# Performance work log

Hardware: AMD Instinct MI355X
Metric: run time of the kernel (lower is better)

## Reference

```python
import jax, jax.numpy as jnp
import numpy as np

N = 4096      # mesh nodes (seq len)
D = 512       # input_dim_nodes / hidden_size
F = 512       # ffn_hidden_size (hidden_dim)
NH = 4        # num_attention_heads
HD = D // NH  # head dim = 128
L = 2         # processor_layers
EPS = 1e-5
SCALE = 1.0 / float(np.sqrt(HD))
NEG = -1e9


def setup_inputs() -> dict:
    key = jax.random.key(0)
    ks = jax.random.split(key, 16)
    nfeat = jax.random.normal(ks[0], (N, D), jnp.float32)
    # sparse graph adjacency mask: True = masked out (TE 'arbitrary' convention)
    mask = jax.random.uniform(ks[1], (N, N)) < 0.99
    idx = jnp.arange(N)
    mask = mask.at[idx, idx].set(False)  # keep self-edges unmasked
    s = 0.02
    p = lambda k, shape: jax.random.normal(k, shape, jnp.float32) * s
    return dict(
        nfeat=nfeat, mask=mask,
        ln1_g=jnp.ones((L, D), jnp.float32), ln1_b=jnp.zeros((L, D), jnp.float32),
        wq=p(ks[2], (L, D, D)), bq=p(ks[3], (L, D)),
        wk=p(ks[4], (L, D, D)), bk=p(ks[5], (L, D)),
        wv=p(ks[6], (L, D, D)), bv=p(ks[7], (L, D)),
        wo=p(ks[8], (L, D, D)), bo=p(ks[9], (L, D)),
        ln2_g=jnp.ones((L, D), jnp.float32), ln2_b=jnp.zeros((L, D), jnp.float32),
        fc1_w=p(ks[10], (L, F, D)), fc1_b=p(ks[11], (L, F)),
        fc2_w=p(ks[12], (L, D, F)), fc2_b=p(ks[13], (L, D)),
    )


def _ln(x, g, b):
    mu = x.mean(-1, keepdims=True)
    var = ((x - mu) ** 2).mean(-1, keepdims=True)
    return (x - mu) * jax.lax.rsqrt(var + EPS) * g + b


def reference(nfeat, mask, ln1_g, ln1_b, wq, bq, wk, bk, wv, bv, wo, bo,
              ln2_g, ln2_b, fc1_w, fc1_b, fc2_w, fc2_b):
    def layer(x, p):
        g1, b1, Wq, Bq, Wk, Bk, Wv, Bv, Wo, Bo, g2, b2, W1, B1, W2, B2 = p
        # --- pre-LN self-attention with arbitrary mask ---
        h = _ln(x, g1, b1)                                  # [N, D]
        q = (h @ Wq.T + Bq).reshape(N, NH, HD)
        k = (h @ Wk.T + Bk).reshape(N, NH, HD)
        v = (h @ Wv.T + Bv).reshape(N, NH, HD)
        scores = jnp.einsum('qhd,khd->hqk', q, k) * SCALE   # [NH, N, N]
        scores = jnp.where(mask[None], NEG, scores)
        attn = jax.nn.softmax(scores, axis=-1)
        o = jnp.einsum('hqk,khd->qhd', attn, v).reshape(N, D)
        x = x + o @ Wo.T + Bo
        # --- pre-LN MLP ---
        h2 = _ln(x, g2, b2)
        m = jax.nn.gelu(h2 @ W1.T + B1, approximate=False) @ W2.T + B2
        return x + m, None

    xs = (ln1_g, ln1_b, wq, bq, wk, bk, wv, bv, wo, bo,
          ln2_g, ln2_b, fc1_w, fc1_b, fc2_w, fc2_b)
    out, _ = jax.lax.scan(layer, nfeat, xs)
    return out
```

## Files before the change

kernel.cpp:

```cpp
#include <hip/hip_runtime.h>
#include <math.h>

#define NN 4096
#define DD 512
#define FF 512
#define CAP 256
#define SCALE 0.08838834764831845f

typedef unsigned short u16;
typedef __attribute__((ext_vector_type(8))) short short8;
typedef __attribute__((ext_vector_type(8))) unsigned short ushort8;
typedef __attribute__((ext_vector_type(4))) unsigned short ushort4v;
typedef __attribute__((ext_vector_type(4))) float floatx4;

__device__ __forceinline__ float bf2f(u16 u) {
    union { unsigned int i; float f; } x; x.i = ((unsigned int)u) << 16; return x.f;
}
__device__ __forceinline__ u16 f2bf(float f) {
    union { float f; unsigned int i; } x; x.f = f;
    unsigned int r = (x.i + 0x7FFFu + ((x.i >> 16) & 1u)) >> 16;
    return (u16)r;
}
__device__ __forceinline__ void gld_lds16(const void* g, void* l) {
    __builtin_amdgcn_global_load_lds((const __attribute__((address_space(1))) void*)g,
                                     (__attribute__((address_space(3))) void*)l, 16, 0, 0);
}

__global__ void build_idx_kernel(const int* __restrict__ mask,
                                 int* __restrict__ idx, int* __restrict__ cnt) {
    int row = blockIdx.x;
    __shared__ int c;
    if (threadIdx.x == 0) c = 0;
    __syncthreads();
    const int4* mrow = (const int4*)(mask + (size_t)row * NN);
    for (int j4 = threadIdx.x; j4 < NN / 4; j4 += blockDim.x) {
        int4 m4 = mrow[j4];
        int base = j4 * 4;
        if (m4.x == 0) idx[row * CAP + atomicAdd(&c, 1)] = base;
        if (m4.y == 0) idx[row * CAP + atomicAdd(&c, 1)] = base + 1;
        if (m4.z == 0) idx[row * CAP + atomicAdd(&c, 1)] = base + 2;
        if (m4.w == 0) idx[row * CAP + atomicAdd(&c, 1)] = base + 3;
    }
    __syncthreads();
    if (threadIdx.x == 0) cnt[row] = (c < CAP) ? c : CAP;
}

struct W6 { const float* w[6]; };
__global__ void cast_weights(W6 wp, u16* __restrict__ dst) {
    int region = blockIdx.x >> 4;
    int layer = region / 6, mat = region - layer * 6;
    const float* src = wp.w[mat] + (size_t)layer * (DD * DD);
    u16* d = dst + (size_t)region * (DD * DD);
    int off = (blockIdx.x & 15) * 16384 + threadIdx.x * 4;
#pragma unroll
    for (int i = 0; i < 16; i++) {
        int e = off + i * 1024;
        float4 f = *(const float4*)&src[e];
        ushort4v u;
        u.x = f2bf(f.x); u.y = f2bf(f.y); u.z = f2bf(f.z); u.w = f2bf(f.w);
        *(ushort4v*)&d[e] = u;
    }
}

__global__ void concat_bias(const float* __restrict__ bq, const float* __restrict__ bk,
                            const float* __restrict__ bv, float* __restrict__ bcat) {
    int l = blockIdx.x, t = threadIdx.x;
    bcat[l * 1536 + t]        = bq[l * 512 + t];
    bcat[l * 1536 + 512 + t]  = bk[l * 512 + t];
    bcat[l * 1536 + 1024 + t] = bv[l * 512 + t];
}

__global__ void ln_kernel(const float* __restrict__ x, const float* __restrict__ g,
                          const float* __restrict__ b, u16* __restrict__ out) {
    int wave = threadIdx.x >> 6, lane = threadIdx.x & 63;
    int row = blockIdx.x * 4 + wave;
    const float* xr = x + (size_t)row * DD;
    float4 p0 = *(const float4*)&xr[lane * 8];
    float4 p1 = *(const float4*)&xr[lane * 8 + 4];
    float v[8] = {p0.x, p0.y, p0.z, p0.w, p1.x, p1.y, p1.z, p1.w};
    float s = 0.f;
#pragma unroll
    for (int i = 0; i < 8; i++) s += v[i];
#pragma unroll
    for (int off = 32; off; off >>= 1) s += __shfl_xor(s, off);
    float mu = s * (1.0f / DD);
    float vs = 0.f;
#pragma unroll
    for (int i = 0; i < 8; i++) { float d = v[i] - mu; vs += d * d; }
#pragma unroll
    for (int off = 32; off; off >>= 1) vs += __shfl_xor(vs, off);
    float r = rsqrtf(vs * (1.0f / DD) + 1e-5f);
    float4 g0 = *(const float4*)&g[lane * 8];
    float4 g1 = *(const float4*)&g[lane * 8 + 4];
    float4 b0 = *(const float4*)&b[lane * 8];
    float4 b1 = *(const float4*)&b[lane * 8 + 4];
    float ge[8] = {g0.x, g0.y, g0.z, g0.w, g1.x, g1.y, g1.z, g1.w};
    float be[8] = {b0.x, b0.y, b0.z, b0.w, b1.x, b1.y, b1.z, b1.w};
    ushort8 ov;
#pragma unroll
    for (int i = 0; i < 8; i++) ov[i] = f2bf((v[i] - mu) * r * ge[i] + be[i]);
    *(ushort8*)&out[(size_t)row * DD + lane * 8] = ov;
}

template <int MODE>
__launch_bounds__(256)
__global__ void gemm_bf16(const u16* __restrict__ A, const u16* __restrict__ B,
                          const float* __restrict__ bias, const float* __restrict__ resIn,
                          float* __restrict__ resOut, u16* __restrict__ outB,
                          int M, int Nout, int K) {
    __shared__ u16 As[64 * 32];
    __shared__ u16 Bs[64 * 32];
    const int m0 = blockIdx.y * 64, n0 = blockIdx.x * 64;
    const int t = threadIdx.x;
    const int wave = t >> 6, lane = t & 63;
    const int wm = (wave & 1) * 32, wn = (wave >> 1) * 32;
    const int srow = t >> 2, scol = (t & 3) * 8;
    const int fr = lane & 15, fq = (lane >> 4) * 8;

    floatx4 acc[2][2] = {};
    const u16* ag = A + (size_t)(m0 + srow) * K + scol;
    const u16* bg = B + (size_t)(n0 + srow) * K + scol;
    u16* as = As + t * 8;
    u16* bs = Bs + t * 8;

    for (int k0 = 0; k0 < K; k0 += 32) {
        __syncthreads();
        gld_lds16(ag + k0, as);
        gld_lds16(bg + k0, bs);
        __syncthreads();
        short8 af[2], bf[2];
#pragma unroll
        for (int i = 0; i < 2; i++) af[i] = *(const short8*)&As[(wm + 16 * i + fr) * 32 + fq];
#pragma unroll
        for (int j = 0; j < 2; j++) bf[j] = *(const short8*)&Bs[(wn + 16 * j + fr) * 32 + fq];
#pragma unroll
        for (int i = 0; i < 2; i++)
#pragma unroll
            for (int j = 0; j < 2; j++)
                acc[i][j] = __builtin_amdgcn_mfma_f32_16x16x32_bf16(af[i], bf[j], acc[i][j], 0, 0, 0);
    }

    const int er = (lane >> 4) * 4, ec = lane & 15;
#pragma unroll
    for (int i = 0; i < 2; i++) {
#pragma unroll
        for (int j = 0; j < 2; j++) {
            int col = n0 + wn + 16 * j + ec;
            float bsv = bias[col];
#pragma unroll
            for (int r = 0; r < 4; r++) {
                int row = m0 + wm + 16 * i + er + r;
                float val = acc[i][j][r] + bsv;
                if (MODE == 1) val = 0.5f * val * (1.0f + erff(val * 0.70710678118654752f));
                if (MODE == 2) {
                    resOut[(size_t)row * Nout + col] = resIn[(size_t)row * Nout + col] + val;
                } else {
                    outB[(size_t)row * Nout + col] = f2bf(val);
                }
            }
        }
    }
}

__launch_bounds__(256)
__global__ void gemm_qkv(const u16* __restrict__ A, const u16* __restrict__ B,
                         const float* __restrict__ bias, u16* __restrict__ outB) {
    __shared__ u16 As[128 * 32];
    __shared__ u16 Bs[64 * 32];
    const int m0 = blockIdx.y * 128, n0 = blockIdx.x * 64;
    const int t = threadIdx.x;
    const int wave = t >> 6, lane = t & 63;
    const int wm = (wave & 1) * 64, wn = (wave >> 1) * 32;
    const int srow = t >> 2, scol = (t & 3) * 8;
    const int fr = lane & 15, fq = (lane >> 4) * 8;

    floatx4 acc[4][2] = {};
    const u16* ag0 = A + (size_t)(m0 + srow) * DD + scol;
    const u16* ag1 = ag0 + (size_t)64 * DD;
    const u16* bg = B + (size_t)(n0 + srow) * DD + scol;
    u16* as0 = As + t * 8;
    u16* as1 = as0 + 64 * 32;
    u16* bs = Bs + t * 8;

    for (int k0 = 0; k0 < DD; k0 += 32) {
        __syncthreads();
        gld_lds16(ag0 + k0, as0);
        gld_lds16(ag1 + k0, as1);
        gld_lds16(bg + k0, bs);
        __syncthreads();
        short8 af[4], bf[2];
#pragma unroll
        for (int i = 0; i < 4; i++) af[i] = *(const short8*)&As[(wm + 16 * i + fr) * 32 + fq];
#pragma unroll
        for (int j = 0; j < 2; j++) bf[j] = *(const short8*)&Bs[(wn + 16 * j + fr) * 32 + fq];
#pragma unroll
        for (int i = 0; i < 4; i++)
#pragma unroll
            for (int j = 0; j < 2; j++)
                acc[i][j] = __builtin_amdgcn_mfma_f32_16x16x32_bf16(af[i], bf[j], acc[i][j], 0, 0, 0);
    }

    const int er = (lane >> 4) * 4, ec = lane & 15;
#pragma unroll
    for (int j = 0; j < 2; j++) {
        int col = n0 + wn + 16 * j + ec;
        float bsv = bias[col];
#pragma unroll
        for (int i = 0; i < 4; i++) {
#pragma unroll
            for (int r = 0; r < 4; r++) {
                int row = m0 + wm + 16 * i + er + r;
                outB[(size_t)row * 1536 + col] = f2bf(acc[i][j][r] + bsv);
            }
        }
    }
}

__global__ void sparse_attn(const u16* __restrict__ qkv, const int* __restrict__ idx,
                            const int* __restrict__ cnt, u16* __restrict__ o) {
    int t = threadIdx.x;
    int wave = t >> 6, lane = t & 63;
    int qslot = wave >> 1, half = wave & 1;
    int qi = blockIdx.x * 4 + qslot;
    __shared__ float obuf[4][64][8];
    __shared__ float sbuf[4][64];
    __shared__ int sidx[4][CAP];

    int c = cnt[qi];
    const int* ir = idx + qi * CAP;
    for (int j = t & 127; j < c; j += 128) sidx[qslot][j] = ir[j];

    ushort8 qv = *(const ushort8*)(qkv + (size_t)qi * 1536 + lane * 8);
    float qf[8];
#pragma unroll
    for (int e = 0; e < 8; e++) qf[e] = bf2f(qv[e]);
    __syncthreads();

    float sum = 0.f, oa[8] = {};
    int j = half;
    ushort8 kv, vv;
    if (j < c) {
        const u16* kb = qkv + (size_t)sidx[qslot][j] * 1536;
        kv = *(const ushort8*)(kb + 512 + lane * 8);
        vv = *(const ushort8*)(kb + 1024 + lane * 8);
    }
    while (j < c) {
        int jn = j + 2;
        ushort8 kvn, vvn;
        {
            int kjn = (jn < c) ? sidx[qslot][jn] : 0;
            const u16* nb = qkv + (size_t)kjn * 1536;
            kvn = *(const ushort8*)(nb + 512 + lane * 8);
            vvn = *(const ushort8*)(nb + 1024 + lane * 8);
        }
        float d = 0.f;
#pragma unroll
        for (int e = 0; e < 8; e++) d += qf[e] * bf2f(kv[e]);
        d += __shfl_xor(d, 1);
        d += __shfl_xor(d, 2);
        d += __shfl_xor(d, 4);
        d += __shfl_xor(d, 8);
        float p = __expf(d * SCALE);
        sum += p;
#pragma unroll
        for (int e = 0; e < 8; e++) oa[e] += p * bf2f(vv[e]);
        kv = kvn; vv = vvn;
        j = jn;
    }

    if (half == 1) {
#pragma unroll
        for (int e = 0; e < 8; e++) obuf[qslot][lane][e] = oa[e];
        sbuf[qslot][lane] = sum;
    }
    __syncthreads();
    if (half == 0) {
        sum += sbuf[qslot][lane];
        float inv = 1.0f / sum;
        ushort8 ov;
#pragma unroll
        for (int e = 0; e < 8; e++) ov[e] = f2bf((oa[e] + obuf[qslot][lane][e]) * inv);
        *(ushort8*)(o + (size_t)qi * 512 + lane * 8) = ov;
    }
}

extern "C" void kernel_launch(void* const* d_in, const int* in_sizes, int n_in,
                              void* d_out, int out_size, void* d_ws, size_t ws_size,
                              hipStream_t stream) {
    const float* nfeat = (const float*)d_in[0];
    const int*   mask  = (const int*)d_in[1];
    const float* ln1_g = (const float*)d_in[2];
    const float* ln1_b = (const float*)d_in[3];
    const float* bo    = (const float*)d_in[11];
    const float* ln2_g = (const float*)d_in[12];
    const float* ln2_b = (const float*)d_in[13];
    const float* fc1_b = (const float*)d_in[15];
    const float* fc2_b = (const float*)d_in[17];

    const size_t ND = (size_t)NN * DD;
    float* x    = (float*)d_ws;
    u16*   h    = (u16*)(x + ND);
    u16*   qkv  = h + ND;
    u16*   o    = qkv + (size_t)NN * 1536;
    u16*   m1   = o + ND;
    u16*   wc   = m1 + ND;
    float* bcat = (float*)(wc + (size_t)12 * DD * DD);
    int*   idx  = (int*)(bcat + 2 * 1536);
    int*   cnt  = idx + (size_t)NN * CAP;

    W6 w6;
    w6.w[0] = (const float*)d_in[4];  w6.w[1] = (const float*)d_in[6];
    w6.w[2] = (const float*)d_in[8];  w6.w[3] = (const float*)d_in[10];
    w6.w[4] = (const float*)d_in[14]; w6.w[5] = (const float*)d_in[16];
    cast_weights<<<192, 256, 0, stream>>>(w6, wc);
    concat_bias<<<2, 512, 0, stream>>>((const float*)d_in[5], (const float*)d_in[7],
                                       (const float*)d_in[9], bcat);
    build_idx_kernel<<<NN, 256, 0, stream>>>(mask, idx, cnt);

    const size_t SS = (size_t)DD * DD;
    for (int l = 0; l < 2; l++) {
        size_t bOff = (size_t)l * DD;
        u16* wl = wc + (size_t)l * 6 * SS;
        const float* xin = (l == 0) ? nfeat : x;
        float* fc2_dst = (l == 1) ? (float*)d_out : x;

        ln_kernel<<<NN / 4, 256, 0, stream>>>(xin, ln1_g + bOff, ln1_b + bOff, h);
        gemm_qkv<<<dim3(24, 32), 256, 0, stream>>>(h, wl, bcat + l * 1536, qkv);
        sparse_attn<<<NN / 4, 512, 0, stream>>>(qkv, idx, cnt, o);
        gemm_bf16<2><<<dim3(8, 64), 256, 0, stream>>>(o, wl + 3 * SS, bo + bOff,
                                                      xin, x, nullptr, NN, DD, DD);
        ln_kernel<<<NN / 4, 256, 0, stream>>>(x, ln2_g + bOff, ln2_b + bOff, h);
        gemm_bf16<1><<<dim3(8, 64), 256, 0, stream>>>(h, wl + 4 * SS, fc1_b + bOff,
                                                      nullptr, nullptr, m1, NN, FF, DD);
        gemm_bf16<2><<<dim3(8, 64), 256, 0, stream>>>(m1, wl + 5 * SS, fc2_b + bOff,
                                                      x, fc2_dst, nullptr, NN, DD, FF);
    }
}
```

Baseline: 293.6 us.

## Swizzle GEMM LDS layout, batch sparse-attention K/V loads, fold bias concat

Result: slower. 315.3 us (+7.4%).

```diff
diff --git a/kernel.cpp b/kernel.cpp
--- a/kernel.cpp
+++ b/kernel.cpp
@@ -45,8 +45,11 @@
     if (threadIdx.x == 0) cnt[row] = (c < CAP) ? c : CAP;
 }
 
-struct W6 { const float* w[6]; };
-__global__ void cast_weights(W6 wp, u16* __restrict__ dst) {
+struct W6 {
+    const float* w[6];
+    const float* bq; const float* bk; const float* bv;
+};
+__global__ void cast_weights(W6 wp, u16* __restrict__ dst, float* __restrict__ bcat) {
     int region = blockIdx.x >> 4;
     int layer = region / 6, mat = region - layer * 6;
     const float* src = wp.w[mat] + (size_t)layer * (DD * DD);
@@ -60,14 +63,15 @@
         u.x = f2bf(f.x); u.y = f2bf(f.y); u.z = f2bf(f.z); u.w = f2bf(f.w);
         *(ushort4v*)&d[e] = u;
     }
-}
-
-__global__ void concat_bias(const float* __restrict__ bq, const float* __restrict__ bk,
-                            const float* __restrict__ bv, float* __restrict__ bcat) {
-    int l = blockIdx.x, t = threadIdx.x;
-    bcat[l * 1536 + t]        = bq[l * 512 + t];
-    bcat[l * 1536 + 512 + t]  = bk[l * 512 + t];
-    bcat[l * 1536 + 1024 + t] = bv[l * 512 + t];
+    if (blockIdx.x < 2) {
+        int l = blockIdx.x;
+        for (int it = 0; it < 6; it++) {
+            int j = it * 256 + threadIdx.x;
+            int m = j >> 9, col = j & 511;
+            const float* bp = (m == 0) ? wp.bq : (m == 1) ? wp.bk : wp.bv;
+            bcat[l * 1536 + j] = bp[l * DD + col];
+        }
+    }
 }
 
 __global__ void ln_kernel(const float* __restrict__ x, const float* __restrict__ g,
@@ -101,6 +105,7 @@
     for (int i = 0; i < 8; i++) ov[i] = f2bf((v[i] - mu) * r * ge[i] + be[i]);
     *(ushort8*)&out[(size_t)row * DD + lane * 8] = ov;
 }
+
 
 template <int MODE>
 __launch_bounds__(256)
@@ -114,8 +119,10 @@
     const int t = threadIdx.x;
     const int wave = t >> 6, lane = t & 63;
     const int wm = (wave & 1) * 32, wn = (wave >> 1) * 32;
-    const int srow = t >> 2, scol = (t & 3) * 8;
-    const int fr = lane & 15, fq = (lane >> 4) * 8;
+    const int srow = t >> 2;
+    const int scol = (((t & 3) + (t >> 3)) & 3) * 8;
+    const int fr = lane & 15, g = lane >> 4;
+    const int fp = ((g - (fr >> 1)) & 3) * 8;
 
     floatx4 acc[2][2] = {};
     const u16* ag = A + (size_t)(m0 + srow) * K + scol;
@@ -130,9 +137,9 @@
         __syncthreads();
         short8 af[2], bf[2];
 #pragma unroll
-        for (int i = 0; i < 2; i++) af[i] = *(const short8*)&As[(wm + 16 * i + fr) * 32 + fq];
-#pragma unroll
-        for (int j = 0; j < 2; j++) bf[j] = *(const short8*)&Bs[(wn + 16 * j + fr) * 32 + fq];
+        for (int i = 0; i < 2; i++) af[i] = *(const short8*)&As[(wm + 16 * i + fr) * 32 + fp];
+#pragma unroll
+        for (int j = 0; j < 2; j++) bf[j] = *(const short8*)&Bs[(wn + 16 * j + fr) * 32 + fp];
 #pragma unroll
         for (int i = 0; i < 2; i++)
 #pragma unroll
@@ -171,8 +178,10 @@
     const int t = threadIdx.x;
     const int wave = t >> 6, lane = t & 63;
     const int wm = (wave & 1) * 64, wn = (wave >> 1) * 32;
-    const int srow = t >> 2, scol = (t & 3) * 8;
-    const int fr = lane & 15, fq = (lane >> 4) * 8;
+    const int srow = t >> 2;
+    const int scol = (((t & 3) + (t >> 3)) & 3) * 8;
+    const int fr = lane & 15, g = lane >> 4;
+    const int fp = ((g - (fr >> 1)) & 3) * 8;
 
     floatx4 acc[4][2] = {};
     const u16* ag0 = A + (size_t)(m0 + srow) * DD + scol;
@@ -190,9 +199,9 @@
         __syncthreads();
         short8 af[4], bf[2];
 #pragma unroll
-        for (int i = 0; i < 4; i++) af[i] = *(const short8*)&As[(wm + 16 * i + fr) * 32 + fq];
-#pragma unroll
-        for (int j = 0; j < 2; j++) bf[j] = *(const short8*)&Bs[(wn + 16 * j + fr) * 32 + fq];
+        for (int i = 0; i < 4; i++) af[i] = *(const short8*)&As[(wm + 16 * i + fr) * 32 + fp];
+#pragma unroll
+        for (int j = 0; j < 2; j++) bf[j] = *(const short8*)&Bs[(wn + 16 * j + fr) * 32 + fp];
 #pragma unroll
         for (int i = 0; i < 4; i++)
 #pragma unroll
@@ -237,35 +246,32 @@
     __syncthreads();
 
     float sum = 0.f, oa[8] = {};
-    int j = half;
-    ushort8 kv, vv;
-    if (j < c) {
-        const u16* kb = qkv + (size_t)sidx[qslot][j] * 1536;
-        kv = *(const ushort8*)(kb + 512 + lane * 8);
-        vv = *(const ushort8*)(kb + 1024 + lane * 8);
-    }
-    while (j < c) {
-        int jn = j + 2;
-        ushort8 kvn, vvn;
-        {
-            int kjn = (jn < c) ? sidx[qslot][jn] : 0;
-            const u16* nb = qkv + (size_t)kjn * 1536;
-            kvn = *(const ushort8*)(nb + 512 + lane * 8);
-            vvn = *(const ushort8*)(nb + 1024 + lane * 8);
-        }
-        float d = 0.f;
-#pragma unroll
-        for (int e = 0; e < 8; e++) d += qf[e] * bf2f(kv[e]);
-        d += __shfl_xor(d, 1);
-        d += __shfl_xor(d, 2);
-        d += __shfl_xor(d, 4);
-        d += __shfl_xor(d, 8);
-        float p = __expf(d * SCALE);
-        sum += p;
-#pragma unroll
-        for (int e = 0; e < 8; e++) oa[e] += p * bf2f(vv[e]);
-        kv = kvn; vv = vvn;
-        j = jn;
+    for (int jb = half; jb < c; jb += 8) {
+        ushort8 kv[4], vv[4];
+#pragma unroll
+        for (int u = 0; u < 4; u++) {
+            int j = jb + 2 * u;
+            int kj = (j < c) ? sidx[qslot][j] : qi;
+            const u16* kb = qkv + (size_t)kj * 1536;
+            kv[u] = *(const ushort8*)(kb + 512 + lane * 8);
+            vv[u] = *(const ushort8*)(kb + 1024 + lane * 8);
+        }
+#pragma unroll
+        for (int u = 0; u < 4; u++) {
+            int j = jb + 2 * u;
+            if (j >= c) break;
+            float d = 0.f;
+#pragma unroll
+            for (int e = 0; e < 8; e++) d += qf[e] * bf2f(kv[u][e]);
+            d += __shfl_xor(d, 1);
+            d += __shfl_xor(d, 2);
+            d += __shfl_xor(d, 4);
+            d += __shfl_xor(d, 8);
+            float p = __expf(d * SCALE);
+            sum += p;
+#pragma unroll
+            for (int e = 0; e < 8; e++) oa[e] += p * bf2f(vv[u][e]);
+        }
     }
 
     if (half == 1) {
@@ -312,9 +318,8 @@
     w6.w[0] = (const float*)d_in[4];  w6.w[1] = (const float*)d_in[6];
     w6.w[2] = (const float*)d_in[8];  w6.w[3] = (const float*)d_in[10];
     w6.w[4] = (const float*)d_in[14]; w6.w[5] = (const float*)d_in[16];
-    cast_weights<<<192, 256, 0, stream>>>(w6, wc);
-    concat_bias<<<2, 512, 0, stream>>>((const float*)d_in[5], (const float*)d_in[7],
-                                       (const float*)d_in[9], bcat);
+    w6.bq = (const float*)d_in[5]; w6.bk = (const float*)d_in[7]; w6.bv = (const float*)d_in[9];
+    cast_weights<<<192, 256, 0, stream>>>(w6, wc, bcat);
     build_idx_kernel<<<NN, 256, 0, stream>>>(mask, idx, cnt);
 
     const size_t SS = (size_t)DD * DD;
```
